# Performance work log

Measured on AMD Instinct MI355X. Metric: run time of the kernel, lower is better.

## Reference

```python
import jax, jax.numpy as jnp
import numpy as np

EPS = 1e-5

def _gcn_norm(edge_index, num_nodes):
    # add self loops (improved=False -> fill value 1.0), symmetric normalization
    src = jnp.concatenate([edge_index[0], jnp.arange(num_nodes)])
    dst = jnp.concatenate([edge_index[1], jnp.arange(num_nodes)])
    w = jnp.ones(src.shape[0], dtype=jnp.float32)
    deg = jax.ops.segment_sum(w, dst, num_segments=num_nodes)
    dinv = jnp.where(deg > 0, 1.0 / jnp.sqrt(deg), 0.0)
    norm = dinv[src] * dinv[dst]  # [E+N]
    return src, dst, norm

def _gcn_conv(x, W, src, dst, norm, num_nodes):
    h = x @ W                      # [N, out]
    msg = h[src] * norm[:, None]   # gather + scale, [E+N, out]
    return jax.ops.segment_sum(msg, dst, num_segments=num_nodes)

def _bn_relu(x, gamma, beta):
    # BatchNorm1d in training mode: biased batch stats over the node dim
    m = x.mean(axis=0)
    v = x.var(axis=0)
    return jax.nn.relu((x - m) * jax.lax.rsqrt(v + EPS) * gamma + beta)

def setup_inputs() -> dict:
    key = jax.random.key(0)
    ks = jax.random.split(key, 12)
    N, E, D_IN, H, D_OUT, DEPTH = 100000, 1600000, 3, 128, 1, 9
    x = jax.random.normal(ks[0], (N, D_IN), dtype=jnp.float32)
    edge_index = jax.random.randint(ks[1], (2, E), 0, N, dtype=jnp.int64)
    s = 1.0 / np.sqrt(H)
    W0 = jax.random.normal(ks[2], (D_IN, H), jnp.float32) / np.sqrt(D_IN)
    Ws1 = jax.random.normal(ks[3], (DEPTH, H, H), jnp.float32) * s
    g1 = jnp.ones((DEPTH + 1, H), jnp.float32)
    b1 = jnp.zeros((DEPTH + 1, H), jnp.float32)
    Ws2 = jax.random.normal(ks[4], (DEPTH - 1, H, H), jnp.float32) * s
    g2 = jnp.ones((DEPTH - 1, H), jnp.float32)
    b2 = jnp.zeros((DEPTH - 1, H), jnp.float32)
    Wout = jax.random.normal(ks[5], (H, D_OUT), jnp.float32) * s
    return {"x": x, "edge_index": edge_index, "W0": W0, "Ws1": Ws1, "g1": g1,
            "b1": b1, "Ws2": Ws2, "g2": g2, "b2": b2, "Wout": Wout}

def reference(x, edge_index, W0, Ws1, g1, b1, Ws2, g2, b2, Wout):
    N = x.shape[0]
    depth = Ws1.shape[0]  # 9
    src, dst, norm = _gcn_norm(edge_index, N)
    # conv1[0]
    h = _bn_relu(_gcn_conv(x, W0, src, dst, norm, N), g1[0], b1[0])
    xs = [h]
    for i in range(1, depth + 1):
        h = _bn_relu(_gcn_conv(h, Ws1[i - 1], src, dst, norm, N), g1[i], b1[i])
        if i < depth:
            xs.append(h)
    for i in range(depth):
        j = depth - i - 1
        h = h + xs[j]
        if i < depth - 1:
            h = _bn_relu(_gcn_conv(h, Ws2[i], src, dst, norm, N), g2[i], b2[i])
        else:
            h = jax.nn.sigmoid(_gcn_conv(h, Wout, src, dst, norm, N))
    return h
```

## Files before the change

kernel.cpp:

```cpp
#include <hip/hip_runtime.h>
#include <hip/hip_bf16.h>

#define EPSV 1e-5f
#define NSTRIPE 16

typedef unsigned int uint;
typedef unsigned short ushort;
typedef __attribute__((ext_vector_type(8))) __bf16 bf16x8;
typedef __attribute__((ext_vector_type(4))) float f32x4;

static __device__ __forceinline__ float bf2f(ushort u) {
    return __uint_as_float(((uint)u) << 16);
}
static __device__ __forceinline__ ushort f2bf(float f) {
    __hip_bfloat16 h = __float2bfloat16(f);
    return __builtin_bit_cast(ushort, h);
}


static __device__ __forceinline__ float e4m3_dec(unsigned char b) {
    int s = b >> 7, E = (b >> 3) & 15, m = b & 7;
    float v = (E == 0) ? (float)m * 0.001953125f
                       : (float)(8 + m) * 0.125f * exp2f((float)(E - 7));
    return s ? -v : v;
}
static __device__ __forceinline__ unsigned char e4m3_enc(float f) {
    unsigned su = (__float_as_uint(f) >> 24) & 0x80u;
    float a = fabsf(f);
    if (!(a < 448.f)) return (unsigned char)(su | 0x7E);
    if (a < 0.015625f) {
        int m = (int)rintf(a * 512.f);
        return (unsigned char)(su | (m >= 8 ? 0x08 : m));
    }
    int e;
    frexpf(a, &e);
    int E = e - 1 + 7;
    float mant = a * exp2f((float)(1 - e)) - 1.0f;
    int mi = (int)rintf(mant * 8.f);
    if (mi >= 8) { mi = 0; E++; }
    if (E >= 16) return (unsigned char)(su | 0x7E);
    if (E == 15 && mi == 7) mi = 6;
    return (unsigned char)(su | (E << 3) | mi);
}


template <typename T> struct IOV;
template <> struct IOV<float> {
    static __device__ __forceinline__ float2 ld2(const float* p) { return *(const float2*)p; }
    static __device__ __forceinline__ void st2(float* p, float a, float b) {
        *(float2*)p = make_float2(a, b);
    }
    static __device__ __forceinline__ void ld8(const float* p, float* v) {
        float4 a = ((const float4*)p)[0], b = ((const float4*)p)[1];
        v[0] = a.x; v[1] = a.y; v[2] = a.z; v[3] = a.w;
        v[4] = b.x; v[5] = b.y; v[6] = b.z; v[7] = b.w;
    }
    static __device__ __forceinline__ void st8(float* p, const float* v) {
        ((float4*)p)[0] = make_float4(v[0], v[1], v[2], v[3]);
        ((float4*)p)[1] = make_float4(v[4], v[5], v[6], v[7]);
    }
};
template <> struct IOV<ushort> {
    static __device__ __forceinline__ float2 ld2(const ushort* p) {
        uint u = *(const uint*)p;
        return make_float2(bf2f((ushort)u), bf2f((ushort)(u >> 16)));
    }
    static __device__ __forceinline__ void st2(ushort* p, float a, float b) {
        *(uint*)p = (uint)f2bf(a) | ((uint)f2bf(b) << 16);
    }
    static __device__ __forceinline__ void ld8(const ushort* p, float* v) {
        uint4 u = *(const uint4*)p;
        v[0] = bf2f((ushort)u.x); v[1] = bf2f((ushort)(u.x >> 16));
        v[2] = bf2f((ushort)u.y); v[3] = bf2f((ushort)(u.y >> 16));
        v[4] = bf2f((ushort)u.z); v[5] = bf2f((ushort)(u.z >> 16));
        v[6] = bf2f((ushort)u.w); v[7] = bf2f((ushort)(u.w >> 16));
    }
    static __device__ __forceinline__ void st8(ushort* p, const float* v) {
        uint4 u;
        u.x = (uint)f2bf(v[0]) | ((uint)f2bf(v[1]) << 16);
        u.y = (uint)f2bf(v[2]) | ((uint)f2bf(v[3]) << 16);
        u.z = (uint)f2bf(v[4]) | ((uint)f2bf(v[5]) << 16);
        u.w = (uint)f2bf(v[6]) | ((uint)f2bf(v[7]) << 16);
        *(uint4*)p = u;
    }
};
template <> struct IOV<unsigned char> {
    static __device__ __forceinline__ float2 ld2(const unsigned char* p) {
        ushort u = *(const ushort*)p;
        return make_float2(e4m3_dec((unsigned char)u), e4m3_dec((unsigned char)(u >> 8)));
    }
    static __device__ __forceinline__ void st2(unsigned char* p, float a, float b) {
        *(ushort*)p = (ushort)e4m3_enc(a) | ((ushort)e4m3_enc(b) << 8);
    }
    static __device__ __forceinline__ void ld8(const unsigned char* p, float* v) {
        uint2 u = *(const uint2*)p;
#pragma unroll
        for (int j = 0; j < 4; j++) v[j] = e4m3_dec((unsigned char)(u.x >> (8 * j)));
#pragma unroll
        for (int j = 0; j < 4; j++) v[4 + j] = e4m3_dec((unsigned char)(u.y >> (8 * j)));
    }
    static __device__ __forceinline__ void st8(unsigned char* p, const float* v) {
        uint2 u = {0, 0};
#pragma unroll
        for (int j = 0; j < 4; j++) u.x |= (uint)e4m3_enc(v[j]) << (8 * j);
#pragma unroll
        for (int j = 0; j < 4; j++) u.y |= (uint)e4m3_enc(v[4 + j]) << (8 * j);
        *(uint2*)p = u;
    }
};


__global__ void k_count(const int* __restrict__ dst, int* __restrict__ cnt, int E) {
    int e = blockIdx.x * blockDim.x + threadIdx.x;
    if (e < E) atomicAdd(&cnt[dst[e]], 1);
}

__global__ void k_scan1(const int* __restrict__ cnt, int* __restrict__ bsum, int N) {
    __shared__ int s[256];
    int i = blockIdx.x * 256 + threadIdx.x;
    s[threadIdx.x] = (i < N) ? ((cnt[i] + 7) & ~7) : 0;
    __syncthreads();
    for (int o = 128; o > 0; o >>= 1) {
        if (threadIdx.x < o) s[threadIdx.x] += s[threadIdx.x + o];
        __syncthreads();
    }
    if (threadIdx.x == 0) bsum[blockIdx.x] = s[0];
}

__global__ void k_scan2(int* __restrict__ bsum, int B) {
    __shared__ int s[1024];
    int t = threadIdx.x;
    int orig = (t < B) ? bsum[t] : 0;
    s[t] = orig;
    __syncthreads();
    for (int o = 1; o < 1024; o <<= 1) {
        int v = (t >= o) ? s[t - o] : 0;
        __syncthreads();
        s[t] += v;
        __syncthreads();
    }
    if (t < B) bsum[t] = s[t] - orig;
}

__global__ void k_scan3(const int* __restrict__ cnt, const int* __restrict__ bsum,
                        int* __restrict__ roff, int* __restrict__ cursor,
                        float* __restrict__ dinv, int N) {
    __shared__ int s[256];
    int i = blockIdx.x * 256 + threadIdx.x;
    int v = (i < N) ? cnt[i] : 0;
    int pv = (v + 7) & ~7;
    s[threadIdx.x] = pv;
    __syncthreads();
    for (int o = 1; o < 256; o <<= 1) {
        int u = (threadIdx.x >= o) ? s[threadIdx.x - o] : 0;
        __syncthreads();
        s[threadIdx.x] += u;
        __syncthreads();
    }
    if (i < N) {
        int off = bsum[blockIdx.x] + s[threadIdx.x] - pv;
        roff[i] = off;
        cursor[i] = off;
        dinv[i] = rsqrtf((float)(v + 1));
        if (i == N - 1) roff[N] = off + pv;
    }
}

__global__ void k_scatter(const int* __restrict__ src, const int* __restrict__ dst,
                          const float* __restrict__ dinv, int* __restrict__ cursor,
                          int2* __restrict__ ev, int E) {
    int e = blockIdx.x * blockDim.x + threadIdx.x;
    if (e < E) {
        int s = src[e], d = dst[e];
        int p = atomicAdd(&cursor[d], 1);
        int2 pk;
        pk.x = s;
        pk.y = __float_as_int(dinv[s] * dinv[d]);
        ev[p] = pk;
    }
}

__global__ void k_pad(const int* __restrict__ cursor, const int* __restrict__ roff,
                      int2* __restrict__ ev, int N) {
    int i = blockIdx.x * blockDim.x + threadIdx.x;
    if (i >= N) return;
    int p = cursor[i], e = roff[i + 1];
    int2 pk;
    pk.x = i;
    pk.y = 0;
    for (; p < e; p++) ev[p] = pk;
}

__global__ void k_prepw(const float* __restrict__ Ws1, const float* __restrict__ Ws2,
                        ushort* __restrict__ whi, ushort* __restrict__ wlo) {
    int idx = blockIdx.x * blockDim.x + threadIdx.x;
    if (idx >= 17 * 16384) return;
    int L = idx >> 14, r = idx & 16383;
    int f = r >> 9, e = r & 511, lane = e >> 3, j = e & 7;
    int n = (f >> 2) * 16 + (lane & 15);
    int k = (f & 3) * 32 + (lane >> 4) * 8 + j;
    const float* W = (L < 9) ? (Ws1 + (size_t)L * 16384) : (Ws2 + (size_t)(L - 9) * 16384);
    float w = W[(size_t)k * 128 + n];
    ushort hi = f2bf(w);
    whi[idx] = hi;
    wlo[idx] = f2bf(w - bf2f(hi));
}


__global__ void k_spmm3(const float* __restrict__ X, const int2* __restrict__ ev,
                        const int* __restrict__ roff, const float* __restrict__ dinv,
                        float* __restrict__ XA, int N) {
    int i = blockIdx.x * blockDim.x + threadIdx.x;
    if (i >= N) return;
    float di = dinv[i];
    float w0 = di * di;
    float a0 = X[(size_t)i * 3 + 0] * w0;
    float a1 = X[(size_t)i * 3 + 1] * w0;
    float a2 = X[(size_t)i * 3 + 2] * w0;
    int je = roff[i + 1];
    for (int j = roff[i]; j < je; j++) {
        int2 e = ev[j];
        float w = __int_as_float(e.y);
        a0 += X[(size_t)e.x * 3 + 0] * w;
        a1 += X[(size_t)e.x * 3 + 1] * w;
        a2 += X[(size_t)e.x * 3 + 2] * w;
    }
    XA[(size_t)i * 3 + 0] = a0;
    XA[(size_t)i * 3 + 1] = a1;
    XA[(size_t)i * 3 + 2] = a2;
}

template <typename ZT>
__global__ __launch_bounds__(256) void k_spmm_stats(
    const ushort* __restrict__ H, const int2* __restrict__ ev,
    const int* __restrict__ roff, const float* __restrict__ dinv,
    ZT* __restrict__ Y, float* __restrict__ st, int N) {
    int lane = threadIdx.x & 63, wv = threadIdx.x >> 6;
    int i = blockIdx.x * 4 + wv;
    const uint* Hu = (const uint*)H;
    float a0 = 0.f, a1 = 0.f;

    if (i < N) {
        float di = dinv[i];
        float ws = di * di;
        uint u = Hu[(size_t)i * 64 + lane];
        a0 = bf2f((ushort)u) * ws;
        a1 = bf2f((ushort)(u >> 16)) * ws;
        int j = roff[i], je = roff[i + 1];
        for (; j < je; j += 8) {
            int2 e0 = ev[j], e1 = ev[j + 1], e2 = ev[j + 2], e3 = ev[j + 3];
            int2 e4 = ev[j + 4], e5 = ev[j + 5], e6 = ev[j + 6], e7 = ev[j + 7];
            uint u0 = Hu[(size_t)e0.x * 64 + lane];
            uint u1 = Hu[(size_t)e1.x * 64 + lane];
            uint u2 = Hu[(size_t)e2.x * 64 + lane];
            uint u3 = Hu[(size_t)e3.x * 64 + lane];
            uint u4 = Hu[(size_t)e4.x * 64 + lane];
            uint u5 = Hu[(size_t)e5.x * 64 + lane];
            uint u6 = Hu[(size_t)e6.x * 64 + lane];
            uint u7 = Hu[(size_t)e7.x * 64 + lane];
            float w0 = __int_as_float(e0.y), w1 = __int_as_float(e1.y);
            float w2 = __int_as_float(e2.y), w3 = __int_as_float(e3.y);
            float w4 = __int_as_float(e4.y), w5 = __int_as_float(e5.y);
            float w6 = __int_as_float(e6.y), w7 = __int_as_float(e7.y);
            a0 += bf2f((ushort)u0) * w0 + bf2f((ushort)u1) * w1 +
                  bf2f((ushort)u2) * w2 + bf2f((ushort)u3) * w3 +
                  bf2f((ushort)u4) * w4 + bf2f((ushort)u5) * w5 +
                  bf2f((ushort)u6) * w6 + bf2f((ushort)u7) * w7;
            a1 += bf2f((ushort)(u0 >> 16)) * w0 + bf2f((ushort)(u1 >> 16)) * w1 +
                  bf2f((ushort)(u2 >> 16)) * w2 + bf2f((ushort)(u3 >> 16)) * w3 +
                  bf2f((ushort)(u4 >> 16)) * w4 + bf2f((ushort)(u5 >> 16)) * w5 +
                  bf2f((ushort)(u6 >> 16)) * w6 + bf2f((ushort)(u7 >> 16)) * w7;
        }
        IOV<ZT>::st2(&Y[(size_t)i * 128 + 2 * lane], a0, a1);
    }

    __shared__ float ls[4][64][4];
    ls[wv][lane][0] = a0; ls[wv][lane][1] = a1;
    ls[wv][lane][2] = a0 * a0; ls[wv][lane][3] = a1 * a1;
    __syncthreads();
    if (wv == 0) {
        float s0 = ls[0][lane][0] + ls[1][lane][0] + ls[2][lane][0] + ls[3][lane][0];
        float s1 = ls[0][lane][1] + ls[1][lane][1] + ls[2][lane][1] + ls[3][lane][1];
        float q0 = ls[0][lane][2] + ls[1][lane][2] + ls[2][lane][2] + ls[3][lane][2];
        float q1 = ls[0][lane][3] + ls[1][lane][3] + ls[2][lane][3] + ls[3][lane][3];
        float* stp = st + (size_t)(blockIdx.x & (NSTRIPE - 1)) * 256;
        atomicAdd(&stp[2 * lane], s0);
        atomicAdd(&stp[2 * lane + 1], s1);
        atomicAdd(&stp[128 + 2 * lane], q0);
        atomicAdd(&stp[129 + 2 * lane], q1);
    }
}

__global__ void k_spmm1(const float* __restrict__ T, const int2* __restrict__ ev,
                        const int* __restrict__ roff, const float* __restrict__ dinv,
                        float* __restrict__ out, int N) {
    int i = blockIdx.x * blockDim.x + threadIdx.x;
    if (i >= N) return;
    float di = dinv[i];
    float a = T[i] * di * di;
    int je = roff[i + 1];
    for (int j = roff[i]; j < je; j++) {
        int2 e = ev[j];
        a += T[e.x] * __int_as_float(e.y);
    }
    out[i] = 1.0f / (1.0f + expf(-a));
}


template <typename ZT>
__global__ __launch_bounds__(256) void k_stats(const ZT* __restrict__ Z,
                                               float* __restrict__ st, int N) {
    int lane = threadIdx.x & 63, rg = threadIdx.x >> 6;
    float s0 = 0.f, s1 = 0.f, q0 = 0.f, q1 = 0.f;
    for (int r = blockIdx.x * 4 + rg; r < N; r += gridDim.x * 4) {
        float2 v = IOV<ZT>::ld2(&Z[(size_t)r * 128 + 2 * lane]);
        s0 += v.x; q0 += v.x * v.x;
        s1 += v.y; q1 += v.y * v.y;
    }
    __shared__ float ls[4][64][4];
    ls[rg][lane][0] = s0; ls[rg][lane][1] = s1;
    ls[rg][lane][2] = q0; ls[rg][lane][3] = q1;
    __syncthreads();
    if (rg == 0) {
        for (int g = 1; g < 4; g++) {
            s0 += ls[g][lane][0]; s1 += ls[g][lane][1];
            q0 += ls[g][lane][2]; q1 += ls[g][lane][3];
        }
        float* stp = st + (size_t)(blockIdx.x & (NSTRIPE - 1)) * 256;
        atomicAdd(&stp[2 * lane], s0);
        atomicAdd(&stp[2 * lane + 1], s1);
        atomicAdd(&stp[128 + 2 * lane], q0);
        atomicAdd(&stp[129 + 2 * lane], q1);
    }
}

__global__ void k_bnfin(const float* __restrict__ st, const float* __restrict__ g,
                        const float* __restrict__ b, float* __restrict__ aff, float invN) {
    int c = threadIdx.x;
    float S = 0.f, Q = 0.f;
    for (int s = 0; s < NSTRIPE; s++) {
        S += st[(size_t)s * 256 + c];
        Q += st[(size_t)s * 256 + 128 + c];
    }
    float m = S * invN;
    float var = Q * invN - m * m;
    float sc = g[c] * rsqrtf(var + EPSV);
    aff[c] = sc;
    aff[128 + c] = b[c] - m * sc;
}


template <typename ZT>
__global__ void k_gemm3(const float* __restrict__ XA, const float* __restrict__ W0,
                        ZT* __restrict__ Y, int N) {
    int idx = blockIdx.x * blockDim.x + threadIdx.x;
    if (idx >= N * 64) return;
    int i = idx >> 6, c0 = (idx & 63) * 2;
    float x0 = XA[(size_t)i * 3], x1 = XA[(size_t)i * 3 + 1], x2 = XA[(size_t)i * 3 + 2];
    float y0 = x0 * W0[c0] + x1 * W0[128 + c0] + x2 * W0[256 + c0];
    float y1 = x0 * W0[c0 + 1] + x1 * W0[128 + c0 + 1] + x2 * W0[256 + c0 + 1];
    IOV<ZT>::st2(&Y[(size_t)i * 128 + c0], y0, y1);
}

template <typename ZT, typename SKT>
__global__ __launch_bounds__(256) void k_gemm_mfma(
    const ZT* __restrict__ Z, const SKT* __restrict__ skip_in, SKT* __restrict__ skip_out,
    const float* __restrict__ st, const float* __restrict__ gz, const float* __restrict__ bz,
    const ushort* __restrict__ whi, const ushort* __restrict__ wlo,
    ushort* __restrict__ H, float invN, int N) {
    __shared__ ushort sW[16384];
    __shared__ float sA[256];
    int tid = threadIdx.x;
    int wave = tid >> 6, lane = tid & 63;
    int l15 = lane & 15, quad = lane >> 4;

    {
        float acc = 0.f;
#pragma unroll
        for (int s = 0; s < NSTRIPE; s++) acc += st[(size_t)s * 256 + tid];
        sA[tid] = acc;
    }
    {
        const uint4* src = (const uint4*)whi;
#pragma unroll
        for (int t = 0; t < 8; t++) ((uint4*)sW)[tid + 256 * t] = src[tid + 256 * t];
    }
    __syncthreads();
    if (tid < 128) {
        float S = sA[tid], Q = sA[128 + tid];
        float m = S * invN;
        float var = Q * invN - m * m;
        float sc = gz[tid] * rsqrtf(var + EPSV);
        sA[tid] = sc;
        sA[128 + tid] = bz[tid] - m * sc;
    }
    __syncthreads();

    int row = blockIdx.x * 64 + wave * 16 + l15;
    size_t rowc = (size_t)(row < N ? row : N - 1);

    bf16x8 ahi[4], alo[4];
#pragma unroll
    for (int kc = 0; kc < 4; kc++) {
        int c0 = kc * 32 + quad * 8;
        float v[8];
        IOV<ZT>::ld8(&Z[rowc * 128 + c0], v);
        float av[8];
#pragma unroll
        for (int jj = 0; jj < 8; jj++) {
            float t = v[jj] * sA[c0 + jj] + sA[128 + c0 + jj];
            av[jj] = fmaxf(t, 0.f);
        }
        if (skip_out && row < N) IOV<SKT>::st8(&skip_out[rowc * 128 + c0], av);
        if (skip_in) {
            float w2[8];
            IOV<SKT>::ld8(&skip_in[rowc * 128 + c0], w2);
#pragma unroll
            for (int jj = 0; jj < 8; jj++) av[jj] += w2[jj];
        }
        bf16x8 fh, fl;
#pragma unroll
        for (int jj = 0; jj < 8; jj++) {
            __bf16 h = (__bf16)av[jj];
            fh[jj] = h;
            fl[jj] = (__bf16)(av[jj] - (float)h);
        }
        ahi[kc] = fh;
        alo[kc] = fl;
    }

    f32x4 acc[8];
#pragma unroll
    for (int ct = 0; ct < 8; ct++) {
        f32x4 z0 = {0.f, 0.f, 0.f, 0.f};
        acc[ct] = z0;
    }

#pragma unroll
    for (int ct = 0; ct < 8; ct++) {
#pragma unroll
        for (int kc = 0; kc < 4; kc++) {
            bf16x8 b = *(const bf16x8*)&sW[(ct * 4 + kc) * 512 + lane * 8];
            acc[ct] = __builtin_amdgcn_mfma_f32_16x16x32_bf16(ahi[kc], b, acc[ct], 0, 0, 0);
            acc[ct] = __builtin_amdgcn_mfma_f32_16x16x32_bf16(alo[kc], b, acc[ct], 0, 0, 0);
        }
    }
    __syncthreads();
    {
        const uint4* src = (const uint4*)wlo;
#pragma unroll
        for (int t = 0; t < 8; t++) ((uint4*)sW)[tid + 256 * t] = src[tid + 256 * t];
    }
    __syncthreads();
#pragma unroll
    for (int ct = 0; ct < 8; ct++) {
#pragma unroll
        for (int kc = 0; kc < 4; kc++) {
            bf16x8 b = *(const bf16x8*)&sW[(ct * 4 + kc) * 512 + lane * 8];
            acc[ct] = __builtin_amdgcn_mfma_f32_16x16x32_bf16(ahi[kc], b, acc[ct], 0, 0, 0);
        }
    }
    __syncthreads();
    ushort* sC = sW;
#pragma unroll
    for (int ct = 0; ct < 8; ct++)
#pragma unroll
        for (int reg = 0; reg < 4; reg++) {
            int r = wave * 16 + quad * 4 + reg;
            sC[r * 136 + ct * 16 + l15] = f2bf(acc[ct][reg]);
        }
    __syncthreads();
    for (int t = tid; t < 1024; t += 256) {
        int r = t >> 4, c4 = t & 15;
        int grow = blockIdx.x * 64 + r;
        if (grow < N)
            ((uint4*)(H + (size_t)grow * 128))[c4] = *(const uint4*)&sC[r * 136 + c4 * 8];
    }
}

template <typename ZT, typename SKT>
__global__ __launch_bounds__(256) void k_dot(
    const ZT* __restrict__ Z, const SKT* __restrict__ S0,
    const float* __restrict__ aff, const float* __restrict__ Wout,
    float* __restrict__ T, int N) {
    int i = blockIdx.x * 4 + (threadIdx.x >> 6);
    if (i >= N) return;
    int lane = threadIdx.x & 63;
    int c0 = 2 * lane, c1 = c0 + 1;
    float2 z = IOV<ZT>::ld2(&Z[(size_t)i * 128 + c0]);
    float2 s = IOV<SKT>::ld2(&S0[(size_t)i * 128 + c0]);
    float p0 = fmaxf(z.x * aff[c0] + aff[128 + c0], 0.f) + s.x;
    float p1 = fmaxf(z.y * aff[c1] + aff[128 + c1], 0.f) + s.y;
    float a = p0 * Wout[c0] + p1 * Wout[c1];
    for (int o = 32; o > 0; o >>= 1) a += __shfl_down(a, o);
    if (lane == 0) T[i] = a;
}


template <typename ZT, typename SKT>
static void run_all(const float* x, const int* src, const int* dst, const float* W0,
                    const float* Ws1, const float* g1, const float* b1,
                    const float* Ws2, const float* g2, const float* b2,
                    const float* Wout, float* out, char* ws, int N, int E,
                    hipStream_t stream) {
    char* p = ws;
    auto alloc = [&](size_t bytes) -> void* {
        void* r = (void*)p;
        p += (bytes + 255) & ~(size_t)255;
        return r;
    };
    size_t Epad = (size_t)E + 7 * (size_t)N + 8;
    int*   roff   = (int*)alloc((size_t)(N + 1) * 4);
    float* dinv   = (float*)alloc((size_t)N * 4);
    int2*  ev     = (int2*)alloc(Epad * 8);
    int*   bsum   = (int*)alloc(4096);
    float* st_all = (float*)alloc((size_t)18 * NSTRIPE * 256 * 4);
    float* aff    = (float*)alloc(1024);
    ushort* whi   = (ushort*)alloc((size_t)17 * 16384 * 2);
    ushort* wlo   = (ushort*)alloc((size_t)17 * 16384 * 2);
    size_t nz = (size_t)N * 128;
    ushort* hb = (ushort*)alloc(nz * 2);
    ZT* zb = (ZT*)alloc(nz * sizeof(ZT));
    SKT* skips = (SKT*)alloc((size_t)9 * nz * sizeof(SKT));
    auto skip = [&](int s) { return skips + (size_t)s * nz; };
    auto stg  = [&](int s) { return st_all + (size_t)s * NSTRIPE * 256; };

    int* cnt    = (int*)skip(8);
    int* cursor = (int*)((char*)skip(8) + (((size_t)N * 4 + 255) & ~(size_t)255));
    float* xa   = (float*)hb;
    float* tbuf = (float*)hb;

    float invN = 1.0f / (float)N;
    auto gb = [&](int stage, const float** g, const float** b) {
        if (stage <= 9) { *g = g1 + (size_t)stage * 128; *b = b1 + (size_t)stage * 128; }
        else { *g = g2 + (size_t)(stage - 10) * 128; *b = b2 + (size_t)(stage - 10) * 128; }
    };

    hipMemsetAsync(st_all, 0, (size_t)18 * NSTRIPE * 256 * 4, stream);
    hipMemsetAsync(cnt, 0, (size_t)N * 4, stream);
    k_count<<<(E + 255) / 256, 256, 0, stream>>>(dst, cnt, E);
    int B = (N + 255) / 256;
    k_scan1<<<B, 256, 0, stream>>>(cnt, bsum, N);
    k_scan2<<<1, 1024, 0, stream>>>(bsum, B);
    k_scan3<<<B, 256, 0, stream>>>(cnt, bsum, roff, cursor, dinv, N);
    k_scatter<<<(E + 255) / 256, 256, 0, stream>>>(src, dst, dinv, cursor, ev, E);
    k_pad<<<(N + 255) / 256, 256, 0, stream>>>(cursor, roff, ev, N);
    k_prepw<<<(17 * 16384 + 255) / 256, 256, 0, stream>>>(Ws1, Ws2, whi, wlo);

    int gg = (N + 63) / 64;
    int gs4 = (N + 3) / 4;

    k_spmm3<<<(N + 255) / 256, 256, 0, stream>>>(x, ev, roff, dinv, xa, N);
    k_gemm3<ZT><<<(N * 64 + 255) / 256, 256, 0, stream>>>(xa, W0, zb, N);
    k_stats<ZT><<<512, 256, 0, stream>>>(zb, stg(0), N);

    for (int l = 1; l <= 9; l++) {
        const float *gzp, *bzp;
        gb(l - 1, &gzp, &bzp);
        k_gemm_mfma<ZT, SKT><<<gg, 256, 0, stream>>>(
            zb, (const SKT*)nullptr, skip(l - 1), stg(l - 1), gzp, bzp,
            whi + (size_t)(l - 1) * 16384, wlo + (size_t)(l - 1) * 16384, hb, invN, N);
        k_spmm_stats<ZT><<<gs4, 256, 0, stream>>>(hb, ev, roff, dinv, zb, stg(l), N);
    }

    for (int i = 0; i < 8; i++) {
        int zs = 9 + i;
        const float *gzp, *bzp;
        gb(zs, &gzp, &bzp);
        k_gemm_mfma<ZT, SKT><<<gg, 256, 0, stream>>>(
            zb, skip(8 - i), (SKT*)nullptr, stg(zs), gzp, bzp,
            whi + (size_t)(9 + i) * 16384, wlo + (size_t)(9 + i) * 16384, hb, invN, N);
        k_spmm_stats<ZT><<<gs4, 256, 0, stream>>>(hb, ev, roff, dinv, zb, stg(10 + i), N);
    }

    const float *gzp, *bzp;
    gb(17, &gzp, &bzp);
    k_bnfin<<<1, 128, 0, stream>>>(stg(17), gzp, bzp, aff, invN);
    k_dot<ZT, SKT><<<gs4, 256, 0, stream>>>(zb, skip(0), aff, Wout, tbuf, N);
    k_spmm1<<<(N + 255) / 256, 256, 0, stream>>>(tbuf, ev, roff, dinv, out, N);
}


extern "C" void kernel_launch(void* const* d_in, const int* in_sizes, int n_in,
                              void* d_out, int out_size, void* d_ws, size_t ws_size,
                              hipStream_t stream) {
    const float* x    = (const float*)d_in[0];
    const int*   ei   = (const int*)d_in[1];
    const float* W0   = (const float*)d_in[2];
    const float* Ws1  = (const float*)d_in[3];
    const float* g1   = (const float*)d_in[4];
    const float* b1   = (const float*)d_in[5];
    const float* Ws2  = (const float*)d_in[6];
    const float* g2   = (const float*)d_in[7];
    const float* b2   = (const float*)d_in[8];
    const float* Wout = (const float*)d_in[9];
    float* out = (float*)d_out;

    int N = in_sizes[0] / 3;
    int E = in_sizes[1] / 2;
    const int* src = ei;
    const int* dst = ei + E;

    size_t nz = (size_t)N * 128;
    size_t Epad = (size_t)E + 7 * (size_t)N + 8;
    auto need = [&](size_t zbytes, size_t skbytes) -> size_t {
        size_t t = 0;
        auto add = [&](size_t b) { t += (b + 255) & ~(size_t)255; };
        add((size_t)(N + 1) * 4);
        add((size_t)N * 4);
        add(Epad * 8);
        add(4096);
        add((size_t)18 * NSTRIPE * 256 * 4);
        add(1024);
        add((size_t)17 * 16384 * 2);
        add((size_t)17 * 16384 * 2);
        add(nz * 2);
        add(nz * zbytes);
        add((size_t)9 * nz * skbytes);
        return t;
    };

    char* ws = (char*)d_ws;
    if (need(4, 2) <= ws_size)
        run_all<float, ushort>(x, src, dst, W0, Ws1, g1, b1, Ws2, g2, b2, Wout, out, ws, N, E, stream);
    else if (need(4, 1) <= ws_size)
        run_all<float, unsigned char>(x, src, dst, W0, Ws1, g1, b1, Ws2, g2, b2, Wout, out, ws, N, E, stream);
    else
        run_all<ushort, unsigned char>(x, src, dst, W0, Ws1, g1, b1, Ws2, g2, b2, Wout, out, ws, N, E, stream);
}
```

Measured before the change: 2.411 ms.

## Drop split-bf16 low MFMA pass, unroll SpMM gather by 16, fuse layer-0 stats

```diff
diff --git a/kernel.cpp b/kernel.cpp
--- a/kernel.cpp
+++ b/kernel.cpp
@@ -118,7 +118,7 @@
 __global__ void k_scan1(const int* __restrict__ cnt, int* __restrict__ bsum, int N) {
     __shared__ int s[256];
     int i = blockIdx.x * 256 + threadIdx.x;
-    s[threadIdx.x] = (i < N) ? ((cnt[i] + 7) & ~7) : 0;
+    s[threadIdx.x] = (i < N) ? ((cnt[i] + 15) & ~15) : 0;
     __syncthreads();
     for (int o = 128; o > 0; o >>= 1) {
         if (threadIdx.x < o) s[threadIdx.x] += s[threadIdx.x + o];
@@ -148,7 +148,7 @@
     __shared__ int s[256];
     int i = blockIdx.x * 256 + threadIdx.x;
     int v = (i < N) ? cnt[i] : 0;
-    int pv = (v + 7) & ~7;
+    int pv = (v + 15) & ~15;
     s[threadIdx.x] = pv;
     __syncthreads();
     for (int o = 1; o < 256; o <<= 1) {
@@ -247,29 +247,19 @@
         a0 = bf2f((ushort)u) * ws;
         a1 = bf2f((ushort)(u >> 16)) * ws;
         int j = roff[i], je = roff[i + 1];
-        for (; j < je; j += 8) {
-            int2 e0 = ev[j], e1 = ev[j + 1], e2 = ev[j + 2], e3 = ev[j + 3];
-            int2 e4 = ev[j + 4], e5 = ev[j + 5], e6 = ev[j + 6], e7 = ev[j + 7];
-            uint u0 = Hu[(size_t)e0.x * 64 + lane];
-            uint u1 = Hu[(size_t)e1.x * 64 + lane];
-            uint u2 = Hu[(size_t)e2.x * 64 + lane];
-            uint u3 = Hu[(size_t)e3.x * 64 + lane];
-            uint u4 = Hu[(size_t)e4.x * 64 + lane];
-            uint u5 = Hu[(size_t)e5.x * 64 + lane];
-            uint u6 = Hu[(size_t)e6.x * 64 + lane];
-            uint u7 = Hu[(size_t)e7.x * 64 + lane];
-            float w0 = __int_as_float(e0.y), w1 = __int_as_float(e1.y);
-            float w2 = __int_as_float(e2.y), w3 = __int_as_float(e3.y);
-            float w4 = __int_as_float(e4.y), w5 = __int_as_float(e5.y);
-            float w6 = __int_as_float(e6.y), w7 = __int_as_float(e7.y);
-            a0 += bf2f((ushort)u0) * w0 + bf2f((ushort)u1) * w1 +
-                  bf2f((ushort)u2) * w2 + bf2f((ushort)u3) * w3 +
-                  bf2f((ushort)u4) * w4 + bf2f((ushort)u5) * w5 +
-                  bf2f((ushort)u6) * w6 + bf2f((ushort)u7) * w7;
-            a1 += bf2f((ushort)(u0 >> 16)) * w0 + bf2f((ushort)(u1 >> 16)) * w1 +
-                  bf2f((ushort)(u2 >> 16)) * w2 + bf2f((ushort)(u3 >> 16)) * w3 +
-                  bf2f((ushort)(u4 >> 16)) * w4 + bf2f((ushort)(u5 >> 16)) * w5 +
-                  bf2f((ushort)(u6 >> 16)) * w6 + bf2f((ushort)(u7 >> 16)) * w7;
+        for (; j < je; j += 16) {
+            int2 e[16];
+            uint uu[16];
+#pragma unroll
+            for (int t = 0; t < 16; t++) e[t] = ev[j + t];
+#pragma unroll
+            for (int t = 0; t < 16; t++) uu[t] = Hu[(size_t)e[t].x * 64 + lane];
+#pragma unroll
+            for (int t = 0; t < 16; t++) {
+                float w = __int_as_float(e[t].y);
+                a0 += bf2f((ushort)uu[t]) * w;
+                a1 += bf2f((ushort)(uu[t] >> 16)) * w;
+            }
         }
         IOV<ZT>::st2(&Y[(size_t)i * 128 + 2 * lane], a0, a1);
     }
@@ -306,34 +296,6 @@
     out[i] = 1.0f / (1.0f + expf(-a));
 }
 
-
-template <typename ZT>
-__global__ __launch_bounds__(256) void k_stats(const ZT* __restrict__ Z,
-                                               float* __restrict__ st, int N) {
-    int lane = threadIdx.x & 63, rg = threadIdx.x >> 6;
-    float s0 = 0.f, s1 = 0.f, q0 = 0.f, q1 = 0.f;
-    for (int r = blockIdx.x * 4 + rg; r < N; r += gridDim.x * 4) {
-        float2 v = IOV<ZT>::ld2(&Z[(size_t)r * 128 + 2 * lane]);
-        s0 += v.x; q0 += v.x * v.x;
-        s1 += v.y; q1 += v.y * v.y;
-    }
-    __shared__ float ls[4][64][4];
-    ls[rg][lane][0] = s0; ls[rg][lane][1] = s1;
-    ls[rg][lane][2] = q0; ls[rg][lane][3] = q1;
-    __syncthreads();
-    if (rg == 0) {
-        for (int g = 1; g < 4; g++) {
-            s0 += ls[g][lane][0]; s1 += ls[g][lane][1];
-            q0 += ls[g][lane][2]; q1 += ls[g][lane][3];
-        }
-        float* stp = st + (size_t)(blockIdx.x & (NSTRIPE - 1)) * 256;
-        atomicAdd(&stp[2 * lane], s0);
-        atomicAdd(&stp[2 * lane + 1], s1);
-        atomicAdd(&stp[128 + 2 * lane], q0);
-        atomicAdd(&stp[129 + 2 * lane], q1);
-    }
-}
-
 __global__ void k_bnfin(const float* __restrict__ st, const float* __restrict__ g,
                         const float* __restrict__ b, float* __restrict__ aff, float invN) {
     int c = threadIdx.x;
@@ -351,15 +313,34 @@
 
 
 template <typename ZT>
-__global__ void k_gemm3(const float* __restrict__ XA, const float* __restrict__ W0,
-                        ZT* __restrict__ Y, int N) {
-    int idx = blockIdx.x * blockDim.x + threadIdx.x;
-    if (idx >= N * 64) return;
-    int i = idx >> 6, c0 = (idx & 63) * 2;
-    float x0 = XA[(size_t)i * 3], x1 = XA[(size_t)i * 3 + 1], x2 = XA[(size_t)i * 3 + 2];
-    float y0 = x0 * W0[c0] + x1 * W0[128 + c0] + x2 * W0[256 + c0];
-    float y1 = x0 * W0[c0 + 1] + x1 * W0[128 + c0 + 1] + x2 * W0[256 + c0 + 1];
-    IOV<ZT>::st2(&Y[(size_t)i * 128 + c0], y0, y1);
+__global__ __launch_bounds__(256) void k_gemm3_stats(
+    const float* __restrict__ XA, const float* __restrict__ W0,
+    ZT* __restrict__ Y, float* __restrict__ st, int N) {
+    int lane = threadIdx.x & 63, wv = threadIdx.x >> 6;
+    int i = blockIdx.x * 4 + wv;
+    float y0 = 0.f, y1 = 0.f;
+    if (i < N) {
+        int c0 = lane * 2;
+        float x0 = XA[(size_t)i * 3], x1 = XA[(size_t)i * 3 + 1], x2 = XA[(size_t)i * 3 + 2];
+        y0 = x0 * W0[c0] + x1 * W0[128 + c0] + x2 * W0[256 + c0];
+        y1 = x0 * W0[c0 + 1] + x1 * W0[128 + c0 + 1] + x2 * W0[256 + c0 + 1];
+        IOV<ZT>::st2(&Y[(size_t)i * 128 + c0], y0, y1);
+    }
+    __shared__ float ls[4][64][4];
+    ls[wv][lane][0] = y0; ls[wv][lane][1] = y1;
+    ls[wv][lane][2] = y0 * y0; ls[wv][lane][3] = y1 * y1;
+    __syncthreads();
+    if (wv == 0) {
+        float s0 = ls[0][lane][0] + ls[1][lane][0] + ls[2][lane][0] + ls[3][lane][0];
+        float s1 = ls[0][lane][1] + ls[1][lane][1] + ls[2][lane][1] + ls[3][lane][1];
+        float q0 = ls[0][lane][2] + ls[1][lane][2] + ls[2][lane][2] + ls[3][lane][2];
+        float q1 = ls[0][lane][3] + ls[1][lane][3] + ls[2][lane][3] + ls[3][lane][3];
+        float* stp = st + (size_t)(blockIdx.x & (NSTRIPE - 1)) * 256;
+        atomicAdd(&stp[2 * lane], s0);
+        atomicAdd(&stp[2 * lane + 1], s1);
+        atomicAdd(&stp[128 + 2 * lane], q0);
+        atomicAdd(&stp[129 + 2 * lane], q1);
+    }
 }
 
 template <typename ZT, typename SKT>
@@ -399,7 +380,7 @@
     int row = blockIdx.x * 64 + wave * 16 + l15;
     size_t rowc = (size_t)(row < N ? row : N - 1);
 
-    bf16x8 ahi[4], alo[4];
+    bf16x8 ahi[4];
 #pragma unroll
     for (int kc = 0; kc < 4; kc++) {
         int c0 = kc * 32 + quad * 8;
@@ -418,15 +399,10 @@
 #pragma unroll
             for (int jj = 0; jj < 8; jj++) av[jj] += w2[jj];
         }
-        bf16x8 fh, fl;
-#pragma unroll
-        for (int jj = 0; jj < 8; jj++) {
-            __bf16 h = (__bf16)av[jj];
-            fh[jj] = h;
-            fl[jj] = (__bf16)(av[jj] - (float)h);
-        }
+        bf16x8 fh;
+#pragma unroll
+        for (int jj = 0; jj < 8; jj++) fh[jj] = (__bf16)av[jj];
         ahi[kc] = fh;
-        alo[kc] = fl;
     }
 
     f32x4 acc[8];
@@ -442,7 +418,6 @@
         for (int kc = 0; kc < 4; kc++) {
             bf16x8 b = *(const bf16x8*)&sW[(ct * 4 + kc) * 512 + lane * 8];
             acc[ct] = __builtin_amdgcn_mfma_f32_16x16x32_bf16(ahi[kc], b, acc[ct], 0, 0, 0);
-            acc[ct] = __builtin_amdgcn_mfma_f32_16x16x32_bf16(alo[kc], b, acc[ct], 0, 0, 0);
         }
     }
     __syncthreads();
@@ -509,7 +484,7 @@
         p += (bytes + 255) & ~(size_t)255;
         return r;
     };
-    size_t Epad = (size_t)E + 7 * (size_t)N + 8;
+    size_t Epad = (size_t)E + 15 * (size_t)N + 16;
     int*   roff   = (int*)alloc((size_t)(N + 1) * 4);
     float* dinv   = (float*)alloc((size_t)N * 4);
     int2*  ev     = (int2*)alloc(Epad * 8);
@@ -551,8 +526,7 @@
     int gs4 = (N + 3) / 4;
 
     k_spmm3<<<(N + 255) / 256, 256, 0, stream>>>(x, ev, roff, dinv, xa, N);
-    k_gemm3<ZT><<<(N * 64 + 255) / 256, 256, 0, stream>>>(xa, W0, zb, N);
-    k_stats<ZT><<<512, 256, 0, stream>>>(zb, stg(0), N);
+    k_gemm3_stats<ZT><<<gs4, 256, 0, stream>>>(xa, W0, zb, stg(0), N);
 
     for (int l = 1; l <= 9; l++) {
         const float *gzp, *bzp;
@@ -602,7 +576,7 @@
     const int* dst = ei + E;
 
     size_t nz = (size_t)N * 128;
-    size_t Epad = (size_t)E + 7 * (size_t)N + 8;
+    size_t Epad = (size_t)E + 15 * (size_t)N + 16;
     auto need = [&](size_t zbytes, size_t skbytes) -> size_t {
         size_t t = 0;
         auto add = [&](size_t b) { t += (b + 255) & ~(size_t)255; };
```

Result: no change. 2.412 ms (+0.0%).
